# Optimization experiments

Measured on AMD Instinct MI355X. Metric: run time of the kernel, lower is better.

Reference implementation:

```python
import jax, jax.numpy as jnp
import numpy as np

N_ENT = 100000
N_REL = 200  # directed relations = 2*N_REL
DIM = 200
N_EDGE = 1000000


def rotate(h, r):
    # complex 'rotate' composition: split last dim into (real, imag) halves
    d = h.shape[-1] // 2
    h_re, h_im = h[..., :d], h[..., d:]
    r_re, r_im = r[..., :d], r[..., d:]
    return jnp.concatenate([h_re * r_re - h_im * r_im,
                            h_re * r_im + h_im * r_re], axis=-1)


def setup_inputs() -> dict:
    key = jax.random.key(0)
    ks = jax.random.split(key, 8)
    return {
        "ent_emb": jax.random.normal(ks[0], (N_ENT, DIM), jnp.float32),
        "rel_emb": jax.random.normal(ks[1], (2 * N_REL, DIM), jnp.float32),
        "loop_rel": jax.random.normal(ks[2], (1, DIM), jnp.float32),
        "w_in": jax.random.normal(ks[3], (DIM, DIM), jnp.float32) * (DIM ** -0.5),
        "w_out": jax.random.normal(ks[4], (DIM, DIM), jnp.float32) * (DIM ** -0.5),
        "w_loop": jax.random.normal(ks[5], (DIM, DIM), jnp.float32) * (DIM ** -0.5),
        "bias": jnp.zeros((DIM,), jnp.float32),
        "bn_gamma": jnp.ones((DIM,), jnp.float32),
        "bn_beta": jnp.zeros((DIM,), jnp.float32),
        "edge_index": jax.random.randint(ks[6], (2, N_EDGE), 0, N_ENT, jnp.int64 if jax.config.jax_enable_x64 else jnp.int32),
        "edge_type": jax.random.randint(ks[7], (N_EDGE,), 0, N_REL, jnp.int64 if jax.config.jax_enable_x64 else jnp.int32),
    }


def reference(ent_emb, rel_emb, loop_rel, w_in, w_out, w_loop, bias,
              bn_gamma, bn_beta, edge_index, edge_type):
    n = ent_emb.shape[0]
    num_rel = rel_emb.shape[0] // 2
    src, dst = edge_index[0], edge_index[1]

    def direction(s, d, etype, W):
        # gather -> compose -> transform: [E, DIM]
        msg = rotate(ent_emb[s], rel_emb[etype]) @ W
        # symmetric degree normalization (CompGCN compute_norm)
        deg = jax.ops.segment_sum(jnp.ones_like(s, ent_emb.dtype), d, num_segments=n)
        inv = jnp.where(deg > 0, deg ** -0.5, 0.0)
        norm = inv[d] * inv[s]
        return jax.ops.segment_sum(msg * norm[:, None], d, num_segments=n)

    in_res = direction(src, dst, edge_type, w_in)
    out_res = direction(dst, src, edge_type + num_rel, w_out)  # inverse edges
    loop_res = rotate(ent_emb, loop_rel) @ w_loop

    out = (in_res + out_res + loop_res) * (1.0 / 3.0) + bias
    # BatchNorm1d over entities (training-mode batch stats)
    mean = out.mean(axis=0)
    var = out.var(axis=0)
    out = (out - mean) * jax.lax.rsqrt(var + 1e-5) * bn_gamma + bn_beta
    return jnp.tanh(out)
```

## Files before the change

kernel.cpp:

```cpp
#include <hip/hip_runtime.h>
#include <math.h>
#include <stdint.h>

#define N_ENT   100000
#define DIM     200
#define HD      100
#define N_RELC  200
#define KP      608
#define BM      128
#define BNN     256
#define NT      19
#define MPAD    100096
#define SCAN_B  2048
#define SCAN_NB 49

typedef uint32_t u32;
typedef __attribute__((ext_vector_type(8))) short bf16x8;
typedef __attribute__((ext_vector_type(4))) float f32x4;

__device__ __forceinline__ float invsqrt_pos(float x) {
    return x > 0.f ? (1.f / sqrtf(x)) : 0.f;
}

__device__ __forceinline__ u32 pack_bf16x2(float a, float b) {
    u32 ua = __float_as_uint(a), ub = __float_as_uint(b);
    ua = (ua + 0x7FFFu + ((ua >> 16) & 1u)) >> 16;
    ub = (ub + 0x7FFFu + ((ub >> 16) & 1u)) >> 16;
    return ua | (ub << 16);
}

__device__ __forceinline__ float bf_lo(u32 u) { return __uint_as_float(u << 16); }
__device__ __forceinline__ float bf_hi(u32 u) { return __uint_as_float(u & 0xFFFF0000u); }

__device__ __forceinline__ void lds_cp16(void* lds, const void* g) {
    auto gp = (const __attribute__((address_space(1))) u32*)(uintptr_t)g;
    auto lp = (__attribute__((address_space(3))) u32*)(u32)(uintptr_t)lds;
    __builtin_amdgcn_global_load_lds(gp, lp, 16, 0, 0);
}

__global__ __launch_bounds__(256) void conv_ent_kernel(
        const float* __restrict__ ent, const float* __restrict__ loop_rel,
        ushort* __restrict__ ent16, ushort* __restrict__ Abuf) {
    int row  = (blockIdx.x * blockDim.x + threadIdx.x) >> 6;
    int lane = threadIdx.x & 63;
    if (row >= N_ENT) return;
    u32* Arow = (u32*)(Abuf + (size_t)row * KP);
    if (lane < 50) {
        const float* h = ent + (size_t)row * DIM;
        float2 re = *(const float2*)(h + 2 * lane);
        float2 im = *(const float2*)(h + HD + 2 * lane);
        u32* e32 = (u32*)(ent16 + (size_t)row * DIM);
        e32[lane]      = pack_bf16x2(re.x, re.y);
        e32[50 + lane] = pack_bf16x2(im.x, im.y);
        float2 lre = *(const float2*)(loop_rel + 2 * lane);
        float2 lim = *(const float2*)(loop_rel + HD + 2 * lane);
        float rx = re.x * lre.x - im.x * lim.x;
        float ry = re.y * lre.y - im.y * lim.y;
        float ix = re.x * lim.x + im.x * lre.x;
        float iy = re.y * lim.y + im.y * lre.y;
        Arow[200 + lane] = pack_bf16x2(rx, ry);
        Arow[250 + lane] = pack_bf16x2(ix, iy);
    } else if (lane < 54) {
        Arow[300 + (lane - 50)] = 0u;
    }
}

__global__ __launch_bounds__(256) void conv_rel_kernel(
        const float* __restrict__ src, ushort* __restrict__ dst, int n4) {
    int i = blockIdx.x * blockDim.x + threadIdx.x;
    int stride = gridDim.x * blockDim.x;
    for (; i < n4; i += stride) {
        float4 v = ((const float4*)src)[i];
        uint2 o;
        o.x = pack_bf16x2(v.x, v.y);
        o.y = pack_bf16x2(v.z, v.w);
        ((uint2*)dst)[i] = o;
    }
}

__global__ __launch_bounds__(256) void deg_kernel(
        const int* __restrict__ src, const int* __restrict__ dst,
        int* __restrict__ deg_in, int* __restrict__ deg_out, int n) {
    int i = blockIdx.x * blockDim.x + threadIdx.x;
    int stride = gridDim.x * blockDim.x;
    for (; i < n; i += stride) {
        atomicAdd(&deg_in[dst[i]], 1);
        atomicAdd(&deg_out[src[i]], 1);
    }
}

__global__ __launch_bounds__(256) void scan_part_kernel(
        const int* __restrict__ deg_in, const int* __restrict__ deg_out,
        int* __restrict__ partials) {
    int dir = blockIdx.x >= SCAN_NB;
    int blk = blockIdx.x - dir * SCAN_NB;
    const int* deg = dir ? deg_out : deg_in;
    int t = threadIdx.x;
    int base = blk * SCAN_B + t * 8;
    int s = 0;
#pragma unroll
    for (int u = 0; u < 8; ++u) {
        int i = base + u;
        if (i < N_ENT) s += deg[i];
    }
    __shared__ int red[256];
    red[t] = s;
    __syncthreads();
    for (int d = 128; d > 0; d >>= 1) {
        if (t < d) red[t] += red[t + d];
        __syncthreads();
    }
    if (t == 0) partials[dir * SCAN_NB + blk] = red[0];
}

__global__ void scan_sums_kernel(int* __restrict__ partials,
                                 int* __restrict__ off_in,
                                 int* __restrict__ off_out) {
    int t = threadIdx.x;
    if (t < 2) {
        int* p = partials + t * SCAN_NB;
        int acc = 0;
        for (int i = 0; i < SCAN_NB; ++i) { int v = p[i]; p[i] = acc; acc += v; }
        (t ? off_out : off_in)[N_ENT] = acc;
    }
}

__global__ __launch_bounds__(256) void scan_apply_kernel(
        const int* __restrict__ deg_in, const int* __restrict__ deg_out,
        const int* __restrict__ partials,
        int* __restrict__ off_in, int* __restrict__ off_out,
        int* __restrict__ cur_in, int* __restrict__ cur_out,
        float* __restrict__ inv_in, float* __restrict__ inv_out) {
    int dir = blockIdx.x >= SCAN_NB;
    int blk = blockIdx.x - dir * SCAN_NB;
    const int* deg = dir ? deg_out : deg_in;
    int* off   = dir ? off_out : off_in;
    int* cur   = dir ? cur_out : cur_in;
    float* inv = dir ? inv_out : inv_in;
    int t = threadIdx.x;
    int base = blk * SCAN_B + t * 8;
    int v[8];
    int s = 0;
#pragma unroll
    for (int u = 0; u < 8; ++u) {
        int i = base + u;
        v[u] = (i < N_ENT) ? deg[i] : 0;
        s += v[u];
    }
    __shared__ int red[256];
    red[t] = s;
    __syncthreads();
    for (int d = 1; d < 256; d <<= 1) {
        int x = (t >= d) ? red[t - d] : 0;
        __syncthreads();
        red[t] += x;
        __syncthreads();
    }
    int run = partials[dir * SCAN_NB + blk] + red[t] - s;
#pragma unroll
    for (int u = 0; u < 8; ++u) {
        int i = base + u;
        if (i < N_ENT) {
            off[i] = run;
            cur[i] = run;
            inv[i] = invsqrt_pos((float)v[u]);
            run += v[u];
        }
    }
}

__global__ __launch_bounds__(256) void fill_kernel(
        const int* __restrict__ src, const int* __restrict__ dst,
        const int* __restrict__ etype,
        int* cur_in, int* cur_out,
        u32* __restrict__ csr_in, u32* __restrict__ csr_out, int n) {
    int i = blockIdx.x * blockDim.x + threadIdx.x;
    int stride = gridDim.x * blockDim.x;
    for (; i < n; i += stride) {
        int s = src[i], d = dst[i], t = etype[i];
        int p0 = atomicAdd(&cur_in[d], 1);
        csr_in[p0] = ((u32)s << 8) | (u32)t;
        int p1 = atomicAdd(&cur_out[s], 1);
        csr_out[p1] = ((u32)d << 8) | (u32)t;
    }
}

__global__ __launch_bounds__(256) void prep_bt_kernel(
        const float* __restrict__ w_in, const float* __restrict__ w_out,
        const float* __restrict__ w_loop, ushort* __restrict__ BT) {
    int i = blockIdx.x * 256 + threadIdx.x;
    if (i >= 256 * KP) return;
    int c = i / KP, k = i % KP;
    float v = 0.f;
    if (c < DIM) {
        if (k < 200)      v = w_in[k * DIM + c];
        else if (k < 400) v = w_out[(k - 200) * DIM + c];
        else if (k < 600) v = w_loop[(k - 400) * DIM + c];
    }
    u32 u = __float_as_uint(v);
    u = (u + 0x7FFFu + ((u >> 16) & 1u)) >> 16;
    BT[i] = (ushort)u;
}

__global__ __launch_bounds__(256) void gather_kernel(
        const ushort* __restrict__ ent16, const ushort* __restrict__ rel16,
        const u32* __restrict__ csr_in, const u32* __restrict__ csr_out,
        const int* __restrict__ off_in, const int* __restrict__ off_out,
        const float* __restrict__ inv_in, const float* __restrict__ inv_out,
        ushort* __restrict__ Abuf) {
    int node = (blockIdx.x * blockDim.x + threadIdx.x) >> 6;
    int lane = threadIdx.x & 63;
    if (node >= N_ENT) return;
    const bool act = lane < 50;
    u32* Arow = (u32*)(Abuf + (size_t)node * KP);

#pragma unroll
    for (int dir = 0; dir < 2; ++dir) {
        const u32* csr = dir ? csr_out : csr_in;
        const int* off = dir ? off_out : off_in;
        const float* inv = dir ? inv_out : inv_in;
        const int tofs = dir ? N_RELC : 0;
        float myinv = inv[node];
        float2 are = {0.f, 0.f}, aim = {0.f, 0.f};
        float2 bre = {0.f, 0.f}, bim = {0.f, 0.f};
        int i0 = off[node], i1 = off[node + 1];
        int i = i0;
        for (; i + 1 < i1; i += 2) {
            u32 pk0 = csr[i], pk1 = csr[i + 1];
            int s0 = (int)(pk0 >> 8), t0 = (int)(pk0 & 255u) + tofs;
            int s1 = (int)(pk1 >> 8), t1 = (int)(pk1 & 255u) + tofs;
            float n0 = myinv * inv[s0];
            float n1 = myinv * inv[s1];
            if (act) {
                const u32* h0 = (const u32*)(ent16 + (size_t)s0 * DIM);
                const u32* r0 = (const u32*)(rel16 + (size_t)t0 * DIM);
                const u32* h1 = (const u32*)(ent16 + (size_t)s1 * DIM);
                const u32* r1 = (const u32*)(rel16 + (size_t)t1 * DIM);
                u32 hre0 = h0[lane], him0 = h0[50 + lane];
                u32 rre0 = r0[lane], rim0 = r0[50 + lane];
                u32 hre1 = h1[lane], him1 = h1[50 + lane];
                u32 rre1 = r1[lane], rim1 = r1[50 + lane];
                {
                    float ha = bf_lo(hre0), hb = bf_hi(hre0);
                    float ia = bf_lo(him0), ib = bf_hi(him0);
                    float ra = bf_lo(rre0), rb = bf_hi(rre0);
                    float ja = bf_lo(rim0), jb = bf_hi(rim0);
                    are.x += (ha * ra - ia * ja) * n0;
                    are.y += (hb * rb - ib * jb) * n0;
                    aim.x += (ha * ja + ia * ra) * n0;
                    aim.y += (hb * jb + ib * rb) * n0;
                }
                {
                    float ha = bf_lo(hre1), hb = bf_hi(hre1);
                    float ia = bf_lo(him1), ib = bf_hi(him1);
                    float ra = bf_lo(rre1), rb = bf_hi(rre1);
                    float ja = bf_lo(rim1), jb = bf_hi(rim1);
                    bre.x += (ha * ra - ia * ja) * n1;
                    bre.y += (hb * rb - ib * jb) * n1;
                    bim.x += (ha * ja + ia * ra) * n1;
                    bim.y += (hb * jb + ib * rb) * n1;
                }
            }
        }
        if (i < i1) {
            u32 pk = csr[i];
            int s = (int)(pk >> 8), t = (int)(pk & 255u) + tofs;
            float nrm = myinv * inv[s];
            if (act) {
                const u32* h32 = (const u32*)(ent16 + (size_t)s * DIM);
                const u32* r32 = (const u32*)(rel16 + (size_t)t * DIM);
                u32 hre = h32[lane], him = h32[50 + lane];
                u32 rre = r32[lane], rim = r32[50 + lane];
                float ha = bf_lo(hre), hb = bf_hi(hre);
                float ia = bf_lo(him), ib = bf_hi(him);
                float ra = bf_lo(rre), rb = bf_hi(rre);
                float ja = bf_lo(rim), jb = bf_hi(rim);
                are.x += (ha * ra - ia * ja) * nrm;
                are.y += (hb * rb - ib * jb) * nrm;
                aim.x += (ha * ja + ia * ra) * nrm;
                aim.y += (hb * jb + ib * rb) * nrm;
            }
        }
        if (act) {
            are.x += bre.x; are.y += bre.y;
            aim.x += bim.x; aim.y += bim.y;
            Arow[dir * 100 + lane]      = pack_bf16x2(are.x, are.y);
            Arow[dir * 100 + 50 + lane] = pack_bf16x2(aim.x, aim.y);
        }
    }
}

__global__ __launch_bounds__(512, 4) void gemm_kernel(
        const ushort* __restrict__ A, const ushort* __restrict__ BT,
        const float* __restrict__ bias, float* __restrict__ out,
        float* __restrict__ stats) {
    __shared__ ushort Asm[2][BM * 32];
    __shared__ ushort Bsm[2][BNN * 32];
    __shared__ float sredS[8][4][16];
    __shared__ float sredQ[8][4][16];
    const int tid = threadIdx.x;
    const int row0 = blockIdx.x * BM;
    const int l = tid & 63;
    const int w = tid >> 6;
    const int wm = w >> 2;
    const int wn = w & 3;

    f32x4 acc[4][4];
#pragma unroll
    for (int i = 0; i < 4; ++i)
#pragma unroll
        for (int j = 0; j < 4; ++j)
            acc[i][j] = (f32x4){0.f, 0.f, 0.f, 0.f};

    {
        int r = tid >> 2, s = tid & 3;
        lds_cp16(&Asm[0][tid * 8], A + (size_t)(row0 + r) * KP + s * 8);
#pragma unroll
        for (int j = 0; j < 2; ++j) {
            int c = tid + j * 512;
            int br = c >> 2, bs = c & 3;
            lds_cp16(&Bsm[0][c * 8], BT + (size_t)br * KP + bs * 8);
        }
    }

    int cur = 0;
    for (int ks = 0; ks < NT; ++ks) {
        __syncthreads();
        if (ks + 1 < NT) {
            const int k0 = (ks + 1) * 32;
            int r = tid >> 2, s = tid & 3;
            lds_cp16(&Asm[cur ^ 1][tid * 8], A + (size_t)(row0 + r) * KP + k0 + s * 8);
#pragma unroll
            for (int j = 0; j < 2; ++j) {
                int c = tid + j * 512;
                int br = c >> 2, bs = c & 3;
                lds_cp16(&Bsm[cur ^ 1][c * 8], BT + (size_t)br * KP + k0 + bs * 8);
            }
        }
        const int kq = (l >> 4) * 8;
        const int lr = l & 15;
        bf16x8 aF[4], bF[4];
#pragma unroll
        for (int mf = 0; mf < 4; ++mf)
            aF[mf] = *(const bf16x8*)&Asm[cur][(wm * 64 + mf * 16 + lr) * 32 + kq];
#pragma unroll
        for (int nf = 0; nf < 4; ++nf)
            bF[nf] = *(const bf16x8*)&Bsm[cur][(wn * 64 + nf * 16 + lr) * 32 + kq];
#pragma unroll
        for (int mf = 0; mf < 4; ++mf)
#pragma unroll
            for (int nf = 0; nf < 4; ++nf)
                acc[mf][nf] = __builtin_amdgcn_mfma_f32_16x16x32_bf16(
                        aF[mf], bF[nf], acc[mf][nf], 0, 0, 0);
        cur ^= 1;
    }

    const int lr = l & 15;
    const int rq = (l >> 4) * 4;
    float colS[4], colQ[4];
#pragma unroll
    for (int nf = 0; nf < 4; ++nf) { colS[nf] = 0.f; colQ[nf] = 0.f; }

#pragma unroll
    for (int nf = 0; nf < 4; ++nf) {
        int gcol = wn * 64 + nf * 16 + lr;
        bool cok = gcol < DIM;
        float b = cok ? bias[gcol] : 0.f;
#pragma unroll
        for (int mf = 0; mf < 4; ++mf) {
            int grow0 = row0 + wm * 64 + mf * 16 + rq;
#pragma unroll
            for (int r = 0; r < 4; ++r) {
                int grow = grow0 + r;
                if (grow < N_ENT && cok) {
                    float v = acc[mf][nf][r] * (1.f / 3.f) + b;
                    out[(size_t)grow * DIM + gcol] = v;
                    colS[nf] += v;
                    colQ[nf] += v * v;
                }
            }
        }
    }
#pragma unroll
    for (int nf = 0; nf < 4; ++nf) {
        colS[nf] += __shfl_down(colS[nf], 32);
        colS[nf] += __shfl_down(colS[nf], 16);
        colQ[nf] += __shfl_down(colQ[nf], 32);
        colQ[nf] += __shfl_down(colQ[nf], 16);
    }
    if (l < 16) {
#pragma unroll
        for (int nf = 0; nf < 4; ++nf) {
            sredS[w][nf][l] = colS[nf];
            sredQ[w][nf][l] = colQ[nf];
        }
    }
    __syncthreads();
    if (tid < DIM) {
        int wn_ = tid >> 6, nf_ = (tid >> 4) & 3, lr_ = tid & 15;
        float s = sredS[wn_][nf_][lr_] + sredS[wn_ + 4][nf_][lr_];
        float q = sredQ[wn_][nf_][lr_] + sredQ[wn_ + 4][nf_][lr_];
        atomicAdd(&stats[tid], s);
        atomicAdd(&stats[DIM + tid], q);
    }
}

__global__ void bn_scale_kernel(
        const float* __restrict__ stats, const float* __restrict__ gamma,
        const float* __restrict__ beta, float* __restrict__ ss) {
    int c = threadIdx.x;
    if (c >= DIM) return;
    float mean = stats[c] * (1.f / (float)N_ENT);
    float var  = stats[DIM + c] * (1.f / (float)N_ENT) - mean * mean;
    float scale = gamma[c] / sqrtf(var + 1e-5f);
    ss[c]       = scale;
    ss[DIM + c] = beta[c] - mean * scale;
}

__global__ __launch_bounds__(256) void bn_tanh_kernel(
        float* __restrict__ out, const float* __restrict__ ss) {
    size_t i = (size_t)blockIdx.x * blockDim.x + threadIdx.x;
    size_t stride = (size_t)gridDim.x * blockDim.x;
    const size_t n4 = (size_t)N_ENT * DIM / 4;
    float4* p = (float4*)out;
    for (; i < n4; i += stride) {
        int c = (int)((i * 4) % DIM);
        float4 v = p[i];
        v.x = tanhf(v.x * ss[c]     + ss[DIM + c]);
        v.y = tanhf(v.y * ss[c + 1] + ss[DIM + c + 1]);
        v.z = tanhf(v.z * ss[c + 2] + ss[DIM + c + 2]);
        v.w = tanhf(v.w * ss[c + 3] + ss[DIM + c + 3]);
        p[i] = v;
    }
}

extern "C" void kernel_launch(void* const* d_in, const int* in_sizes, int n_in,
                              void* d_out, int out_size, void* d_ws, size_t ws_size,
                              hipStream_t stream) {
    const float* ent      = (const float*)d_in[0];
    const float* rel      = (const float*)d_in[1];
    const float* loop_rel = (const float*)d_in[2];
    const float* w_in     = (const float*)d_in[3];
    const float* w_out    = (const float*)d_in[4];
    const float* w_loop   = (const float*)d_in[5];
    const float* bias     = (const float*)d_in[6];
    const float* gamma    = (const float*)d_in[7];
    const float* beta     = (const float*)d_in[8];
    const int*   eidx     = (const int*)d_in[9];
    const int*   etype    = (const int*)d_in[10];
    const int n_edge = in_sizes[10];
    const int* src = eidx;
    const int* dst = eidx + n_edge;

    ushort* Abuf   = (ushort*)d_ws;
    ushort* BT     = Abuf + (size_t)MPAD * KP;
    int* deg_in    = (int*)(BT + 256 * KP);
    int* deg_out   = deg_in + N_ENT;
    int* off_in    = deg_out + N_ENT;
    int* off_out   = off_in + N_ENT + 1;
    int* cur_in    = off_out + N_ENT + 1;
    int* cur_out   = cur_in + N_ENT;
    float* inv_in  = (float*)(cur_out + N_ENT);
    float* inv_out = inv_in + N_ENT;
    int* partials  = (int*)(inv_out + N_ENT);
    u32* csr_in    = (u32*)(partials + 2 * SCAN_NB);
    u32* csr_out   = csr_in + n_edge;
    float* stats   = (float*)(csr_out + n_edge);
    float* ss      = stats + 2 * DIM;
    ushort* rel16  = (ushort*)(ss + 2 * DIM);
    float* outp    = (float*)d_out;
    ushort* ent16  = (ushort*)d_out;

    hipMemsetAsync(deg_in, 0, (size_t)2 * N_ENT * sizeof(int), stream);
    hipMemsetAsync(stats, 0, (size_t)2 * DIM * sizeof(float), stream);

    conv_ent_kernel<<<(N_ENT * 64 + 255) / 256, 256, 0, stream>>>(
        ent, loop_rel, ent16, Abuf);
    conv_rel_kernel<<<79, 256, 0, stream>>>(rel, rel16, 2 * N_RELC * DIM / 4);
    deg_kernel<<<2048, 256, 0, stream>>>(src, dst, deg_in, deg_out, n_edge);
    scan_part_kernel<<<2 * SCAN_NB, 256, 0, stream>>>(deg_in, deg_out, partials);
    scan_sums_kernel<<<1, 64, 0, stream>>>(partials, off_in, off_out);
    scan_apply_kernel<<<2 * SCAN_NB, 256, 0, stream>>>(
        deg_in, deg_out, partials, off_in, off_out, cur_in, cur_out,
        inv_in, inv_out);
    fill_kernel<<<2048, 256, 0, stream>>>(src, dst, etype, cur_in, cur_out,
                                          csr_in, csr_out, n_edge);
    prep_bt_kernel<<<(256 * KP + 255) / 256, 256, 0, stream>>>(w_in, w_out, w_loop, BT);
    gather_kernel<<<25000, 256, 0, stream>>>(ent16, rel16, csr_in, csr_out,
                                             off_in, off_out, inv_in, inv_out, Abuf);
    gemm_kernel<<<MPAD / BM, 512, 0, stream>>>(Abuf, BT, bias, outp, stats);
    bn_scale_kernel<<<1, 256, 0, stream>>>(stats, gamma, beta, ss);
    bn_tanh_kernel<<<2048, 256, 0, stream>>>(outp, ss);
}
```

Baseline: 594.7 us.

## Fold scan-sum and BN-scale kernels into consumers; unroll gather loop by four

Removes the single-thread scan_sums kernel by having each scan_apply block sum the preceding partials itself and write the final offset. It also removes bn_scale_kernel by computing the per-channel scale and shift into shared memory at the start of every bn_tanh block. The gather loop is unrolled from two to four edges with independent accumulators, so more loads are in flight per wavefront. Together these cut two tiny launches and raise memory-level parallelism, at the cost of redundant per-block work and more registers in the gather kernel.

```diff
diff --git a/kernel.cpp b/kernel.cpp
--- a/kernel.cpp
+++ b/kernel.cpp
@@ -113,18 +113,6 @@
     if (t == 0) partials[dir * SCAN_NB + blk] = red[0];
 }
 
-__global__ void scan_sums_kernel(int* __restrict__ partials,
-                                 int* __restrict__ off_in,
-                                 int* __restrict__ off_out) {
-    int t = threadIdx.x;
-    if (t < 2) {
-        int* p = partials + t * SCAN_NB;
-        int acc = 0;
-        for (int i = 0; i < SCAN_NB; ++i) { int v = p[i]; p[i] = acc; acc += v; }
-        (t ? off_out : off_in)[N_ENT] = acc;
-    }
-}
-
 __global__ __launch_bounds__(256) void scan_apply_kernel(
         const int* __restrict__ deg_in, const int* __restrict__ deg_out,
         const int* __restrict__ partials,
@@ -156,7 +144,9 @@
         red[t] += x;
         __syncthreads();
     }
-    int run = partials[dir * SCAN_NB + blk] + red[t] - s;
+    int base_off = 0;
+    for (int b = 0; b < blk; ++b) base_off += partials[dir * SCAN_NB + b];
+    int run = base_off + red[t] - s;
 #pragma unroll
     for (int u = 0; u < 8; ++u) {
         int i = base + u;
@@ -165,6 +155,7 @@
             cur[i] = run;
             inv[i] = invsqrt_pos((float)v[u]);
             run += v[u];
+            if (i == N_ENT - 1) off[N_ENT] = run;
         }
     }
 }
@@ -223,23 +214,38 @@
         float myinv = inv[node];
         float2 are = {0.f, 0.f}, aim = {0.f, 0.f};
         float2 bre = {0.f, 0.f}, bim = {0.f, 0.f};
+        float2 cre = {0.f, 0.f}, cim = {0.f, 0.f};
+        float2 dre = {0.f, 0.f}, dim_ = {0.f, 0.f};
         int i0 = off[node], i1 = off[node + 1];
         int i = i0;
-        for (; i + 1 < i1; i += 2) {
-            u32 pk0 = csr[i], pk1 = csr[i + 1];
+        for (; i + 3 < i1; i += 4) {
+            u32 pk0 = csr[i],     pk1 = csr[i + 1];
+            u32 pk2 = csr[i + 2], pk3 = csr[i + 3];
             int s0 = (int)(pk0 >> 8), t0 = (int)(pk0 & 255u) + tofs;
             int s1 = (int)(pk1 >> 8), t1 = (int)(pk1 & 255u) + tofs;
+            int s2 = (int)(pk2 >> 8), t2 = (int)(pk2 & 255u) + tofs;
+            int s3 = (int)(pk3 >> 8), t3 = (int)(pk3 & 255u) + tofs;
             float n0 = myinv * inv[s0];
             float n1 = myinv * inv[s1];
+            float n2 = myinv * inv[s2];
+            float n3 = myinv * inv[s3];
             if (act) {
                 const u32* h0 = (const u32*)(ent16 + (size_t)s0 * DIM);
                 const u32* r0 = (const u32*)(rel16 + (size_t)t0 * DIM);
                 const u32* h1 = (const u32*)(ent16 + (size_t)s1 * DIM);
                 const u32* r1 = (const u32*)(rel16 + (size_t)t1 * DIM);
+                const u32* h2 = (const u32*)(ent16 + (size_t)s2 * DIM);
+                const u32* r2 = (const u32*)(rel16 + (size_t)t2 * DIM);
+                const u32* h3 = (const u32*)(ent16 + (size_t)s3 * DIM);
+                const u32* r3 = (const u32*)(rel16 + (size_t)t3 * DIM);
                 u32 hre0 = h0[lane], him0 = h0[50 + lane];
                 u32 rre0 = r0[lane], rim0 = r0[50 + lane];
                 u32 hre1 = h1[lane], him1 = h1[50 + lane];
                 u32 rre1 = r1[lane], rim1 = r1[50 + lane];
+                u32 hre2 = h2[lane], him2 = h2[50 + lane];
+                u32 rre2 = r2[lane], rim2 = r2[50 + lane];
+                u32 hre3 = h3[lane], him3 = h3[50 + lane];
+                u32 rre3 = r3[lane], rim3 = r3[50 + lane];
                 {
                     float ha = bf_lo(hre0), hb = bf_hi(hre0);
                     float ia = bf_lo(him0), ib = bf_hi(him0);
@@ -260,9 +266,29 @@
                     bim.x += (ha * ja + ia * ra) * n1;
                     bim.y += (hb * jb + ib * rb) * n1;
                 }
+                {
+                    float ha = bf_lo(hre2), hb = bf_hi(hre2);
+                    float ia = bf_lo(him2), ib = bf_hi(him2);
+                    float ra = bf_lo(rre2), rb = bf_hi(rre2);
+                    float ja = bf_lo(rim2), jb = bf_hi(rim2);
+                    cre.x += (ha * ra - ia * ja) * n2;
+                    cre.y += (hb * rb - ib * jb) * n2;
+                    cim.x += (ha * ja + ia * ra) * n2;
+                    cim.y += (hb * jb + ib * rb) * n2;
+                }
+                {
+                    float ha = bf_lo(hre3), hb = bf_hi(hre3);
+                    float ia = bf_lo(him3), ib = bf_hi(him3);
+                    float ra = bf_lo(rre3), rb = bf_hi(rre3);
+                    float ja = bf_lo(rim3), jb = bf_hi(rim3);
+                    dre.x += (ha * ra - ia * ja) * n3;
+                    dre.y += (hb * rb - ib * jb) * n3;
+                    dim_.x += (ha * ja + ia * ra) * n3;
+                    dim_.y += (hb * jb + ib * rb) * n3;
+                }
             }
         }
-        if (i < i1) {
+        for (; i < i1; ++i) {
             u32 pk = csr[i];
             int s = (int)(pk >> 8), t = (int)(pk & 255u) + tofs;
             float nrm = myinv * inv[s];
@@ -282,8 +308,10 @@
             }
         }
         if (act) {
-            are.x += bre.x; are.y += bre.y;
-            aim.x += bim.x; aim.y += bim.y;
+            are.x += bre.x + cre.x + dre.x;
+            are.y += bre.y + cre.y + dre.y;
+            aim.x += bim.x + cim.x + dim_.x;
+            aim.y += bim.y + cim.y + dim_.y;
             Arow[dir * 100 + lane]      = pack_bf16x2(are.x, are.y);
             Arow[dir * 100 + 50 + lane] = pack_bf16x2(aim.x, aim.y);
         }
@@ -405,20 +433,19 @@
     }
 }
 
-__global__ void bn_scale_kernel(
-        const float* __restrict__ stats, const float* __restrict__ gamma,
-        const float* __restrict__ beta, float* __restrict__ ss) {
-    int c = threadIdx.x;
-    if (c >= DIM) return;
-    float mean = stats[c] * (1.f / (float)N_ENT);
-    float var  = stats[DIM + c] * (1.f / (float)N_ENT) - mean * mean;
-    float scale = gamma[c] / sqrtf(var + 1e-5f);
-    ss[c]       = scale;
-    ss[DIM + c] = beta[c] - mean * scale;
-}
-
 __global__ __launch_bounds__(256) void bn_tanh_kernel(
-        float* __restrict__ out, const float* __restrict__ ss) {
+        float* __restrict__ out, const float* __restrict__ stats,
+        const float* __restrict__ gamma, const float* __restrict__ beta) {
+    __shared__ float ssc[DIM], ssh[DIM];
+    int t = threadIdx.x;
+    if (t < DIM) {
+        float mean = stats[t] * (1.f / (float)N_ENT);
+        float var  = stats[DIM + t] * (1.f / (float)N_ENT) - mean * mean;
+        float scale = gamma[t] / sqrtf(var + 1e-5f);
+        ssc[t] = scale;
+        ssh[t] = beta[t] - mean * scale;
+    }
+    __syncthreads();
     size_t i = (size_t)blockIdx.x * blockDim.x + threadIdx.x;
     size_t stride = (size_t)gridDim.x * blockDim.x;
     const size_t n4 = (size_t)N_ENT * DIM / 4;
@@ -426,10 +453,10 @@
     for (; i < n4; i += stride) {
         int c = (int)((i * 4) % DIM);
         float4 v = p[i];
-        v.x = tanhf(v.x * ss[c]     + ss[DIM + c]);
-        v.y = tanhf(v.y * ss[c + 1] + ss[DIM + c + 1]);
-        v.z = tanhf(v.z * ss[c + 2] + ss[DIM + c + 2]);
-        v.w = tanhf(v.w * ss[c + 3] + ss[DIM + c + 3]);
+        v.x = tanhf(v.x * ssc[c]     + ssh[c]);
+        v.y = tanhf(v.y * ssc[c + 1] + ssh[c + 1]);
+        v.z = tanhf(v.z * ssc[c + 2] + ssh[c + 2]);
+        v.w = tanhf(v.w * ssc[c + 3] + ssh[c + 3]);
         p[i] = v;
     }
 }
@@ -466,8 +493,7 @@
     u32* csr_in    = (u32*)(partials + 2 * SCAN_NB);
     u32* csr_out   = csr_in + n_edge;
     float* stats   = (float*)(csr_out + n_edge);
-    float* ss      = stats + 2 * DIM;
-    ushort* rel16  = (ushort*)(ss + 2 * DIM);
+    ushort* rel16  = (ushort*)(stats + 2 * DIM);
     float* outp    = (float*)d_out;
     ushort* ent16  = (ushort*)d_out;
 
@@ -479,7 +505,6 @@
     conv_rel_kernel<<<79, 256, 0, stream>>>(rel, rel16, 2 * N_RELC * DIM / 4);
     deg_kernel<<<2048, 256, 0, stream>>>(src, dst, deg_in, deg_out, n_edge);
     scan_part_kernel<<<2 * SCAN_NB, 256, 0, stream>>>(deg_in, deg_out, partials);
-    scan_sums_kernel<<<1, 64, 0, stream>>>(partials, off_in, off_out);
     scan_apply_kernel<<<2 * SCAN_NB, 256, 0, stream>>>(
         deg_in, deg_out, partials, off_in, off_out, cur_in, cur_out,
         inv_in, inv_out);
@@ -489,6 +514,5 @@
     gather_kernel<<<25000, 256, 0, stream>>>(ent16, rel16, csr_in, csr_out,
                                              off_in, off_out, inv_in, inv_out, Abuf);
     gemm_kernel<<<MPAD / BM, 512, 0, stream>>>(Abuf, BT, bias, outp, stats);
-    bn_scale_kernel<<<1, 256, 0, stream>>>(stats, gamma, beta, ss);
-    bn_tanh_kernel<<<2048, 256, 0, stream>>>(outp, ss);
-}
+    bn_tanh_kernel<<<2048, 256, 0, stream>>>(outp, stats, gamma, beta);
+}
```

New measurement: 568.6 us. -4.4%, faster.
